# Kernel tuning notes

Measured on AMD Instinct MI355X. Metric: run time of the kernel, lower is better.

Reference implementation:

```python
import jax, jax.numpy as jnp
import numpy as np


def setup_inputs() -> dict:
    key = jax.random.key(0)
    k1, k2 = jax.random.split(key)
    d_feat, n, out_dim = 4096, 8192, 2048
    x = jax.random.normal(k1, (d_feat, n), dtype=jnp.float32)
    Psi = jax.random.normal(k2, (out_dim, n), dtype=jnp.float32)
    return {"x": x, "Psi": Psi}


def reference(x, Psi):
    # Original: out = Psi @ H @ x.T @ x with H = I_n - (1/n) * ones(n, n).
    # Psi @ H subtracts the row-mean of Psi (centering over the sample axis),
    # which is mathematically identical but avoids materializing the n x n H.
    Psi_c = Psi - jnp.mean(Psi, axis=1, keepdims=True)        # [out_dim, n]
    tmp = jnp.einsum('on,dn->od', Psi_c, x)                   # Psi_c @ x.T -> [out_dim, d]
    out = jnp.einsum('od,dn->on', tmp, x)                     # @ x -> [out_dim, n]
    return out
```

## Files before the change

### kernel.cpp

```cpp
#include <hip/hip_runtime.h>
#include <cstdint>
#include <cstddef>


typedef __bf16 bf16x8 __attribute__((ext_vector_type(8)));
typedef float f32x4 __attribute__((ext_vector_type(4)));

__device__ __forceinline__ unsigned short f2bf(float f) {
  unsigned u = __builtin_bit_cast(unsigned, f);
  u += 0x7FFFu + ((u >> 16) & 1u);
  return (unsigned short)(u >> 16);
}

__device__ __forceinline__ void gload_lds16(const void* g, void* l) {
  __builtin_amdgcn_global_load_lds(
      (const __attribute__((address_space(1))) unsigned int*)g,
      (__attribute__((address_space(3))) unsigned int*)l, 16, 0, 0);
}

__device__ __forceinline__ void barrier_nofence() {
  asm volatile("" ::: "memory");
  __builtin_amdgcn_s_barrier();
  asm volatile("" ::: "memory");
}
#define WAIT_LGKM0()                                   \
  do {                                                 \
    asm volatile("s_waitcnt lgkmcnt(0)" ::: "memory"); \
    __builtin_amdgcn_sched_barrier(0);                 \
  } while (0)

template <int MH, int NH, int MFR2>
__device__ __forceinline__ void mma_quad(f32x4 (&acc)[2 * MFR2][4],
                                         const bf16x8 (&aF)[MFR2][2],
                                         const bf16x8 (&bF)[2][2]) {
#pragma unroll
  for (int f = 0; f < MFR2; ++f)
#pragma unroll
    for (int g = 0; g < 2; ++g)
#pragma unroll
      for (int kk = 0; kk < 2; ++kk)
        acc[MH * MFR2 + f][NH * 2 + g] = __builtin_amdgcn_mfma_f32_16x16x32_bf16(
            aF[f][kk], bF[g][kk], acc[MH * MFR2 + f][NH * 2 + g], 0, 0, 0);
}

template <int BM, typename OutT>
__global__ __launch_bounds__(512, 2) void gemm8p(
    const unsigned short* __restrict__ A, const unsigned short* __restrict__ B,
    OutT* __restrict__ C, int M, int Nc, int K) {
  constexpr int BN = 256, BK = 64;
  constexpr int MFR = BM / 32, MFR2 = MFR / 2;
  constexpr int APLANE = BM * 64;
  constexpr int ABUF = 2 * APLANE;
  constexpr int BPLANE = BN * 64, BBUF = 2 * BPLANE;
  __shared__ __align__(1024) char lds[2 * ABUF + 2 * BBUF];
  char* Al = lds;
  char* Bl = lds + 2 * ABUF;

  const int nwg = gridDim.x * gridDim.y;
  const int wgid = blockIdx.y * gridDim.x + blockIdx.x;
  const int swz = (wgid & 7) * (nwg >> 3) + (wgid >> 3);
  const int bx = swz % gridDim.x, by = swz / gridDim.x;
  const int tileM = by * BM, tileN = bx * BN;

  const int t = threadIdx.x, lane = t & 63, wave = t >> 6;
  const int wm = wave >> 2, wn = wave & 3;
  const int rsel = lane & 15;
  const int cs = (((lane >> 4) ^ (((lane >> 3) & 1) << 1)) << 4);

  const unsigned short* Ag = A + (size_t)tileM * K;
  const unsigned short* Bg = B + (size_t)tileN * K;
  const int cgA = (((t & 3) ^ (((t >> 5) & 1) << 1))) * 8;
  const int NT = K / BK;

  auto stageA = [&](int h, int kt) {
    int b2 = kt & 1;
    if constexpr (BM == 256) {
#pragma unroll
      for (int kk = 0; kk < 2; ++kk) {
        int r = h * 128 + (t >> 2);
        gload_lds16(Ag + (size_t)r * K + kt * 64 + kk * 32 + cgA,
                    Al + b2 * ABUF + kk * APLANE + h * 8192 + t * 16);
      }
    } else {
      int r = h * 64 + ((t >> 2) & 63);
      int kk = t >> 8;
      gload_lds16(Ag + (size_t)r * K + kt * 64 + kk * 32 + cgA,
                  Al + b2 * ABUF + kk * APLANE + h * 4096 + (t & 255) * 16);
    }
  };
  auto stageB = [&](int h, int kt) {
    int b2 = kt & 1;
#pragma unroll
    for (int kk = 0; kk < 2; ++kk) {
      int r = h * 128 + (t >> 2);
      gload_lds16(Bg + (size_t)r * K + kt * 64 + kk * 32 + cgA,
                  Bl + b2 * BBUF + kk * BPLANE + h * 8192 + t * 16);
    }
  };
  auto waitv_steady = [&]() {
    if constexpr (BM == 256)
      asm volatile("s_waitcnt vmcnt(6)" ::: "memory");
    else
      asm volatile("s_waitcnt vmcnt(4)" ::: "memory");
  };

  f32x4 acc[MFR][4] = {};
  bf16x8 aF[MFR2][2], bF[2][2];

  stageA(0, 0); stageB(1, 0); stageA(1, 0); stageB(0, 0);
  stageA(0, 1); stageB(1, 1); stageA(1, 1);
  waitv_steady();
  barrier_nofence();

  for (int kt = 0; kt < NT; ++kt) {
    const char* Ab = Al + (kt & 1) * ABUF;
    const char* Bb = Bl + (kt & 1) * BBUF;
#pragma unroll
    for (int f = 0; f < MFR2; ++f)
#pragma unroll
      for (int kk = 0; kk < 2; ++kk)
        aF[f][kk] = *(const bf16x8*)(Ab + kk * APLANE +
                                     ((2 * f + wm) * 16 + rsel) * 64 + cs);
#pragma unroll
    for (int g = 0; g < 2; ++g)
#pragma unroll
      for (int kk = 0; kk < 2; ++kk)
        bF[g][kk] = *(const bf16x8*)(Bb + kk * BPLANE +
                                     ((4 * g + wn) * 16 + rsel) * 64 + cs);
    if (kt + 1 < NT) stageB(0, kt + 1);
    barrier_nofence();
    WAIT_LGKM0();
    __builtin_amdgcn_s_setprio(1);
    mma_quad<0, 0, MFR2>(acc, aF, bF);
    __builtin_amdgcn_s_setprio(0);
    barrier_nofence();
#pragma unroll
    for (int g = 0; g < 2; ++g)
#pragma unroll
      for (int kk = 0; kk < 2; ++kk)
        bF[g][kk] = *(const bf16x8*)(Bb + kk * BPLANE +
                                     ((4 * (g + 2) + wn) * 16 + rsel) * 64 + cs);
    if (kt + 2 < NT) stageA(0, kt + 2);
    barrier_nofence();
    WAIT_LGKM0();
    __builtin_amdgcn_s_setprio(1);
    mma_quad<0, 1, MFR2>(acc, aF, bF);
    __builtin_amdgcn_s_setprio(0);
    barrier_nofence();
#pragma unroll
    for (int f = 0; f < MFR2; ++f)
#pragma unroll
      for (int kk = 0; kk < 2; ++kk)
        aF[f][kk] = *(const bf16x8*)(Ab + kk * APLANE +
                                     ((2 * (f + MFR2) + wm) * 16 + rsel) * 64 + cs);
    if (kt + 2 < NT) stageB(1, kt + 2);
    barrier_nofence();
    WAIT_LGKM0();
    __builtin_amdgcn_s_setprio(1);
    mma_quad<1, 1, MFR2>(acc, aF, bF);
    __builtin_amdgcn_s_setprio(0);
    barrier_nofence();
#pragma unroll
    for (int g = 0; g < 2; ++g)
#pragma unroll
      for (int kk = 0; kk < 2; ++kk)
        bF[g][kk] = *(const bf16x8*)(Bb + kk * BPLANE +
                                     ((4 * g + wn) * 16 + rsel) * 64 + cs);
    if (kt + 2 < NT) stageA(1, kt + 2);
    barrier_nofence();
    WAIT_LGKM0();
    __builtin_amdgcn_s_setprio(1);
    mma_quad<1, 0, MFR2>(acc, aF, bF);
    __builtin_amdgcn_s_setprio(0);
    if (kt + 2 < NT)
      waitv_steady();
    else
      asm volatile("s_waitcnt vmcnt(0)" ::: "memory");
    barrier_nofence();
  }

#pragma unroll
  for (int f = 0; f < MFR; ++f) {
    int row0 = tileM + (2 * f + wm) * 16 + ((lane >> 4) << 2);
#pragma unroll
    for (int g = 0; g < 4; ++g) {
      int col = tileN + (4 * g + wn) * 16 + rsel;
#pragma unroll
      for (int r = 0; r < 4; ++r) {
        size_t off = (size_t)(row0 + r) * Nc + col;
        if constexpr (__is_same(OutT, float))
          C[off] = acc[f][g][r];
        else
          C[off] = f2bf(acc[f][g][r]);
      }
    }
  }
}

__global__ void center_psi_kernel(const float* __restrict__ Psi,
                                  unsigned short* __restrict__ pc, int N) {
  int row = blockIdx.x;
  const float4* src = (const float4*)(Psi + (size_t)row * N);
  int n4 = N >> 2;
  float s = 0.f;
  for (int i = threadIdx.x; i < n4; i += blockDim.x) {
    float4 v = src[i];
    s += (v.x + v.y) + (v.z + v.w);
  }
#pragma unroll
  for (int off = 32; off > 0; off >>= 1) s += __shfl_down(s, off);
  __shared__ float red[4];
  if ((threadIdx.x & 63) == 0) red[threadIdx.x >> 6] = s;
  __syncthreads();
  float mean = (red[0] + red[1] + red[2] + red[3]) / (float)N;
  ushort4* dst = (ushort4*)(pc + (size_t)row * N);
  for (int i = threadIdx.x; i < n4; i += blockDim.x) {
    float4 v = src[i];
    ushort4 o;
    o.x = f2bf(v.x - mean);
    o.y = f2bf(v.y - mean);
    o.z = f2bf(v.z - mean);
    o.w = f2bf(v.w - mean);
    dst[i] = o;
  }
}

__global__ void ct_kernel(const float* __restrict__ x,
                          unsigned short* __restrict__ xb,
                          unsigned short* __restrict__ xtb, int D, int N) {
  __shared__ float tile[64][65];
  int n0 = blockIdx.x * 64, d0 = blockIdx.y * 64;
  int tx = threadIdx.x, ty = threadIdx.y;
#pragma unroll
  for (int i = 0; i < 16; i++) {
    int d = ty + 4 * i;
    float v = x[(size_t)(d0 + d) * N + n0 + tx];
    tile[d][tx] = v;
    xb[(size_t)(d0 + d) * N + n0 + tx] = f2bf(v);
  }
  __syncthreads();
#pragma unroll
  for (int i = 0; i < 16; i++) {
    int nn = ty + 4 * i;
    xtb[(size_t)(n0 + nn) * D + d0 + tx] = f2bf(tile[tx][nn]);
  }
}

extern "C" void kernel_launch(void* const* d_in, const int* in_sizes, int n_in,
                              void* d_out, int out_size, void* d_ws,
                              size_t ws_size, hipStream_t stream) {
  const int D = 4096, N = 8192, O = 2048;
  const float* x = (const float*)d_in[0];
  const float* Psi = (const float*)d_in[1];
  float* out = (float*)d_out;

  char* ws = (char*)d_ws;
  unsigned short* xb = (unsigned short*)(ws);
  unsigned short* xtb = (unsigned short*)(ws + ((size_t)64 << 20));
  unsigned short* pc = (unsigned short*)(ws + ((size_t)128 << 20));
  unsigned short* tmpb = (unsigned short*)(ws + ((size_t)160 << 20));

  center_psi_kernel<<<O, 256, 0, stream>>>(Psi, pc, N);
  ct_kernel<<<dim3(N / 64, D / 64), dim3(64, 4), 0, stream>>>(x, xb, xtb, D, N);
  gemm8p<128, unsigned short><<<dim3(D / 256, O / 128), 512, 0, stream>>>(
      pc, xb, tmpb, O, D, N);
  gemm8p<256, float><<<dim3(N / 256, O / 256), 512, 0, stream>>>(
      tmpb, xtb, out, O, N, D);
}
```

Before: 523.9 us.

## Fuse preprocessing kernels and restructure both GEMM pipelines

Merges the Psi-centering and the x cast/transpose kernels into a single launch. The transpose now uses float4 loads and a bf16 LDS tile. The first GEMM becomes a 2-phase schedule: it loads all B fragments at once and prefetches the full next k-tile, replacing the 4-phase scheme with its two-ahead A prefetch. The second GEMM is specialized into separate bF0/bF1 fragment registers and reuses bF0 in the last quadrant without an extra LDS read. The changes cut launch count, preprocessing memory traffic and LDS reads, at the cost of higher register pressure and a shallower prefetch in the first GEMM.

```diff
diff --git a/kernel.cpp b/kernel.cpp
--- a/kernel.cpp
+++ b/kernel.cpp
@@ -28,29 +28,13 @@
     asm volatile("s_waitcnt lgkmcnt(0)" ::: "memory"); \
     __builtin_amdgcn_sched_barrier(0);                 \
   } while (0)
-
-template <int MH, int NH, int MFR2>
-__device__ __forceinline__ void mma_quad(f32x4 (&acc)[2 * MFR2][4],
-                                         const bf16x8 (&aF)[MFR2][2],
-                                         const bf16x8 (&bF)[2][2]) {
-#pragma unroll
-  for (int f = 0; f < MFR2; ++f)
-#pragma unroll
-    for (int g = 0; g < 2; ++g)
-#pragma unroll
-      for (int kk = 0; kk < 2; ++kk)
-        acc[MH * MFR2 + f][NH * 2 + g] = __builtin_amdgcn_mfma_f32_16x16x32_bf16(
-            aF[f][kk], bF[g][kk], acc[MH * MFR2 + f][NH * 2 + g], 0, 0, 0);
-}
-
-template <int BM, typename OutT>
-__global__ __launch_bounds__(512, 2) void gemm8p(
+#define WAITV(N) asm volatile("s_waitcnt vmcnt(" #N ")" ::: "memory")
+
+__global__ __launch_bounds__(512, 2) void gemm2p(
     const unsigned short* __restrict__ A, const unsigned short* __restrict__ B,
-    OutT* __restrict__ C, int M, int Nc, int K) {
-  constexpr int BN = 256, BK = 64;
-  constexpr int MFR = BM / 32, MFR2 = MFR / 2;
-  constexpr int APLANE = BM * 64;
-  constexpr int ABUF = 2 * APLANE;
+    unsigned short* __restrict__ C, int M, int Nc, int K) {
+  constexpr int BM = 128, BN = 256;
+  constexpr int APLANE = BM * 64, ABUF = 2 * APLANE;
   constexpr int BPLANE = BN * 64, BBUF = 2 * BPLANE;
   __shared__ __align__(1024) char lds[2 * ABUF + 2 * BBUF];
   char* Al = lds;
@@ -70,23 +54,14 @@
   const unsigned short* Ag = A + (size_t)tileM * K;
   const unsigned short* Bg = B + (size_t)tileN * K;
   const int cgA = (((t & 3) ^ (((t >> 5) & 1) << 1))) * 8;
-  const int NT = K / BK;
+  const int NT = K / 64;
 
   auto stageA = [&](int h, int kt) {
     int b2 = kt & 1;
-    if constexpr (BM == 256) {
-#pragma unroll
-      for (int kk = 0; kk < 2; ++kk) {
-        int r = h * 128 + (t >> 2);
-        gload_lds16(Ag + (size_t)r * K + kt * 64 + kk * 32 + cgA,
-                    Al + b2 * ABUF + kk * APLANE + h * 8192 + t * 16);
-      }
-    } else {
-      int r = h * 64 + ((t >> 2) & 63);
-      int kk = t >> 8;
-      gload_lds16(Ag + (size_t)r * K + kt * 64 + kk * 32 + cgA,
-                  Al + b2 * ABUF + kk * APLANE + h * 4096 + (t & 255) * 16);
-    }
+    int r = h * 64 + ((t >> 2) & 63);
+    int kk = t >> 8;
+    gload_lds16(Ag + (size_t)r * K + kt * 64 + kk * 32 + cgA,
+                Al + b2 * ABUF + kk * APLANE + h * 4096 + (t & 255) * 16);
   };
   auto stageB = [&](int h, int kt) {
     int b2 = kt & 1;
@@ -97,152 +72,286 @@
                   Bl + b2 * BBUF + kk * BPLANE + h * 8192 + t * 16);
     }
   };
-  auto waitv_steady = [&]() {
-    if constexpr (BM == 256)
-      asm volatile("s_waitcnt vmcnt(6)" ::: "memory");
-    else
-      asm volatile("s_waitcnt vmcnt(4)" ::: "memory");
-  };
-
-  f32x4 acc[MFR][4] = {};
-  bf16x8 aF[MFR2][2], bF[2][2];
-
-  stageA(0, 0); stageB(1, 0); stageA(1, 0); stageB(0, 0);
-  stageA(0, 1); stageB(1, 1); stageA(1, 1);
-  waitv_steady();
+
+  f32x4 acc[4][4] = {};
+  bf16x8 aF[2][2], bFall[4][2];
+
+  stageB(0, 0); stageA(0, 0); stageB(1, 0); stageA(1, 0);
+  WAITV(1);
   barrier_nofence();
 
   for (int kt = 0; kt < NT; ++kt) {
     const char* Ab = Al + (kt & 1) * ABUF;
     const char* Bb = Bl + (kt & 1) * BBUF;
 #pragma unroll
-    for (int f = 0; f < MFR2; ++f)
+    for (int f = 0; f < 2; ++f)
 #pragma unroll
       for (int kk = 0; kk < 2; ++kk)
         aF[f][kk] = *(const bf16x8*)(Ab + kk * APLANE +
                                      ((2 * f + wm) * 16 + rsel) * 64 + cs);
 #pragma unroll
-    for (int g = 0; g < 2; ++g)
-#pragma unroll
-      for (int kk = 0; kk < 2; ++kk)
-        bF[g][kk] = *(const bf16x8*)(Bb + kk * BPLANE +
-                                     ((4 * g + wn) * 16 + rsel) * 64 + cs);
-    if (kt + 1 < NT) stageB(0, kt + 1);
-    barrier_nofence();
-    WAIT_LGKM0();
-    __builtin_amdgcn_s_setprio(1);
-    mma_quad<0, 0, MFR2>(acc, aF, bF);
-    __builtin_amdgcn_s_setprio(0);
-    barrier_nofence();
-#pragma unroll
-    for (int g = 0; g < 2; ++g)
-#pragma unroll
-      for (int kk = 0; kk < 2; ++kk)
-        bF[g][kk] = *(const bf16x8*)(Bb + kk * BPLANE +
-                                     ((4 * (g + 2) + wn) * 16 + rsel) * 64 + cs);
-    if (kt + 2 < NT) stageA(0, kt + 2);
-    barrier_nofence();
-    WAIT_LGKM0();
-    __builtin_amdgcn_s_setprio(1);
-    mma_quad<0, 1, MFR2>(acc, aF, bF);
-    __builtin_amdgcn_s_setprio(0);
-    barrier_nofence();
-#pragma unroll
-    for (int f = 0; f < MFR2; ++f)
+    for (int g = 0; g < 4; ++g)
+#pragma unroll
+      for (int kk = 0; kk < 2; ++kk)
+        bFall[g][kk] = *(const bf16x8*)(Bb + kk * BPLANE +
+                                        ((4 * g + wn) * 16 + rsel) * 64 + cs);
+    if (kt + 1 < NT) { stageB(0, kt + 1); stageA(0, kt + 1); }
+    barrier_nofence();
+    WAIT_LGKM0();
+    __builtin_amdgcn_s_setprio(1);
+#pragma unroll
+    for (int f = 0; f < 2; ++f)
+#pragma unroll
+      for (int g = 0; g < 4; ++g)
+#pragma unroll
+        for (int kk = 0; kk < 2; ++kk)
+          acc[f][g] = __builtin_amdgcn_mfma_f32_16x16x32_bf16(
+              aF[f][kk], bFall[g][kk], acc[f][g], 0, 0, 0);
+    __builtin_amdgcn_s_setprio(0);
+    if (kt == NT - 1) { WAITV(0); } else { WAITV(3); }
+    barrier_nofence();
+#pragma unroll
+    for (int f = 0; f < 2; ++f)
 #pragma unroll
       for (int kk = 0; kk < 2; ++kk)
         aF[f][kk] = *(const bf16x8*)(Ab + kk * APLANE +
-                                     ((2 * (f + MFR2) + wm) * 16 + rsel) * 64 + cs);
-    if (kt + 2 < NT) stageB(1, kt + 2);
-    barrier_nofence();
-    WAIT_LGKM0();
-    __builtin_amdgcn_s_setprio(1);
-    mma_quad<1, 1, MFR2>(acc, aF, bF);
-    __builtin_amdgcn_s_setprio(0);
-    barrier_nofence();
-#pragma unroll
-    for (int g = 0; g < 2; ++g)
-#pragma unroll
-      for (int kk = 0; kk < 2; ++kk)
-        bF[g][kk] = *(const bf16x8*)(Bb + kk * BPLANE +
-                                     ((4 * g + wn) * 16 + rsel) * 64 + cs);
-    if (kt + 2 < NT) stageA(1, kt + 2);
-    barrier_nofence();
-    WAIT_LGKM0();
-    __builtin_amdgcn_s_setprio(1);
-    mma_quad<1, 0, MFR2>(acc, aF, bF);
-    __builtin_amdgcn_s_setprio(0);
-    if (kt + 2 < NT)
-      waitv_steady();
-    else
-      asm volatile("s_waitcnt vmcnt(0)" ::: "memory");
-    barrier_nofence();
-  }
-
-#pragma unroll
-  for (int f = 0; f < MFR; ++f) {
+                                     ((2 * (f + 2) + wm) * 16 + rsel) * 64 + cs);
+    if (kt + 1 < NT) { stageB(1, kt + 1); stageA(1, kt + 1); }
+    barrier_nofence();
+    WAIT_LGKM0();
+    __builtin_amdgcn_s_setprio(1);
+#pragma unroll
+    for (int f = 0; f < 2; ++f)
+#pragma unroll
+      for (int g = 0; g < 4; ++g)
+#pragma unroll
+        for (int kk = 0; kk < 2; ++kk)
+          acc[2 + f][g] = __builtin_amdgcn_mfma_f32_16x16x32_bf16(
+              aF[f][kk], bFall[g][kk], acc[2 + f][g], 0, 0, 0);
+    __builtin_amdgcn_s_setprio(0);
+    WAITV(1);
+    barrier_nofence();
+  }
+
+#pragma unroll
+  for (int f = 0; f < 4; ++f) {
     int row0 = tileM + (2 * f + wm) * 16 + ((lane >> 4) << 2);
 #pragma unroll
     for (int g = 0; g < 4; ++g) {
       int col = tileN + (4 * g + wn) * 16 + rsel;
 #pragma unroll
-      for (int r = 0; r < 4; ++r) {
-        size_t off = (size_t)(row0 + r) * Nc + col;
-        if constexpr (__is_same(OutT, float))
-          C[off] = acc[f][g][r];
-        else
-          C[off] = f2bf(acc[f][g][r]);
-      }
-    }
-  }
-}
-
-__global__ void center_psi_kernel(const float* __restrict__ Psi,
-                                  unsigned short* __restrict__ pc, int N) {
-  int row = blockIdx.x;
-  const float4* src = (const float4*)(Psi + (size_t)row * N);
-  int n4 = N >> 2;
-  float s = 0.f;
-  for (int i = threadIdx.x; i < n4; i += blockDim.x) {
-    float4 v = src[i];
-    s += (v.x + v.y) + (v.z + v.w);
-  }
-#pragma unroll
-  for (int off = 32; off > 0; off >>= 1) s += __shfl_down(s, off);
+      for (int r = 0; r < 4; ++r)
+        C[(size_t)(row0 + r) * Nc + col] = f2bf(acc[f][g][r]);
+    }
+  }
+}
+
+__global__ __launch_bounds__(512, 2) void gemm4p(
+    const unsigned short* __restrict__ A, const unsigned short* __restrict__ B,
+    float* __restrict__ C, int M, int Nc, int K) {
+  constexpr int BM = 256, BN = 256;
+  constexpr int APLANE = BM * 64, ABUF = 2 * APLANE;
+  constexpr int BPLANE = BN * 64, BBUF = 2 * BPLANE;
+  __shared__ __align__(1024) char lds[2 * ABUF + 2 * BBUF];
+  char* Al = lds;
+  char* Bl = lds + 2 * ABUF;
+
+  const int nwg = gridDim.x * gridDim.y;
+  const int wgid = blockIdx.y * gridDim.x + blockIdx.x;
+  const int swz = (wgid & 7) * (nwg >> 3) + (wgid >> 3);
+  const int bx = swz % gridDim.x, by = swz / gridDim.x;
+  const int tileM = by * BM, tileN = bx * BN;
+
+  const int t = threadIdx.x, lane = t & 63, wave = t >> 6;
+  const int wm = wave >> 2, wn = wave & 3;
+  const int rsel = lane & 15;
+  const int cs = (((lane >> 4) ^ (((lane >> 3) & 1) << 1)) << 4);
+
+  const unsigned short* Ag = A + (size_t)tileM * K;
+  const unsigned short* Bg = B + (size_t)tileN * K;
+  const int cgA = (((t & 3) ^ (((t >> 5) & 1) << 1))) * 8;
+  const int NT = K / 64;
+
+  auto stageA = [&](int h, int kt) {
+    int b2 = kt & 1;
+#pragma unroll
+    for (int kk = 0; kk < 2; ++kk) {
+      int r = h * 128 + (t >> 2);
+      gload_lds16(Ag + (size_t)r * K + kt * 64 + kk * 32 + cgA,
+                  Al + b2 * ABUF + kk * APLANE + h * 8192 + t * 16);
+    }
+  };
+  auto stageB = [&](int h, int kt) {
+    int b2 = kt & 1;
+#pragma unroll
+    for (int kk = 0; kk < 2; ++kk) {
+      int r = h * 128 + (t >> 2);
+      gload_lds16(Bg + (size_t)r * K + kt * 64 + kk * 32 + cgA,
+                  Bl + b2 * BBUF + kk * BPLANE + h * 8192 + t * 16);
+    }
+  };
+
+  f32x4 acc[8][4] = {};
+  bf16x8 aF[4][2], bF0[2][2], bF1[2][2];
+
+  stageA(0, 0); stageB(1, 0); stageA(1, 0); stageB(0, 0);
+  stageA(0, 1); stageB(1, 1); stageA(1, 1);
+  WAITV(6);
+  barrier_nofence();
+
+  for (int kt = 0; kt < NT; ++kt) {
+    const char* Ab = Al + (kt & 1) * ABUF;
+    const char* Bb = Bl + (kt & 1) * BBUF;
+#pragma unroll
+    for (int f = 0; f < 4; ++f)
+#pragma unroll
+      for (int kk = 0; kk < 2; ++kk)
+        aF[f][kk] = *(const bf16x8*)(Ab + kk * APLANE +
+                                     ((2 * f + wm) * 16 + rsel) * 64 + cs);
+#pragma unroll
+    for (int g = 0; g < 2; ++g)
+#pragma unroll
+      for (int kk = 0; kk < 2; ++kk)
+        bF0[g][kk] = *(const bf16x8*)(Bb + kk * BPLANE +
+                                      ((4 * g + wn) * 16 + rsel) * 64 + cs);
+    if (kt + 1 < NT) stageB(0, kt + 1);
+    barrier_nofence();
+    WAIT_LGKM0();
+    __builtin_amdgcn_s_setprio(1);
+#pragma unroll
+    for (int f = 0; f < 4; ++f)
+#pragma unroll
+      for (int g = 0; g < 2; ++g)
+#pragma unroll
+        for (int kk = 0; kk < 2; ++kk)
+          acc[f][g] = __builtin_amdgcn_mfma_f32_16x16x32_bf16(
+              aF[f][kk], bF0[g][kk], acc[f][g], 0, 0, 0);
+    __builtin_amdgcn_s_setprio(0);
+    barrier_nofence();
+#pragma unroll
+    for (int g = 0; g < 2; ++g)
+#pragma unroll
+      for (int kk = 0; kk < 2; ++kk)
+        bF1[g][kk] = *(const bf16x8*)(Bb + kk * BPLANE +
+                                      ((4 * (g + 2) + wn) * 16 + rsel) * 64 + cs);
+    if (kt + 2 < NT) stageA(0, kt + 2);
+    barrier_nofence();
+    WAIT_LGKM0();
+    __builtin_amdgcn_s_setprio(1);
+#pragma unroll
+    for (int f = 0; f < 4; ++f)
+#pragma unroll
+      for (int g = 0; g < 2; ++g)
+#pragma unroll
+        for (int kk = 0; kk < 2; ++kk)
+          acc[f][2 + g] = __builtin_amdgcn_mfma_f32_16x16x32_bf16(
+              aF[f][kk], bF1[g][kk], acc[f][2 + g], 0, 0, 0);
+    __builtin_amdgcn_s_setprio(0);
+    barrier_nofence();
+#pragma unroll
+    for (int f = 0; f < 4; ++f)
+#pragma unroll
+      for (int kk = 0; kk < 2; ++kk)
+        aF[f][kk] = *(const bf16x8*)(Ab + kk * APLANE +
+                                     ((2 * (f + 4) + wm) * 16 + rsel) * 64 + cs);
+    if (kt + 2 < NT) stageB(1, kt + 2);
+    barrier_nofence();
+    WAIT_LGKM0();
+    __builtin_amdgcn_s_setprio(1);
+#pragma unroll
+    for (int f = 0; f < 4; ++f)
+#pragma unroll
+      for (int g = 0; g < 2; ++g)
+#pragma unroll
+        for (int kk = 0; kk < 2; ++kk)
+          acc[4 + f][2 + g] = __builtin_amdgcn_mfma_f32_16x16x32_bf16(
+              aF[f][kk], bF1[g][kk], acc[4 + f][2 + g], 0, 0, 0);
+    __builtin_amdgcn_s_setprio(0);
+    barrier_nofence();
+    if (kt + 2 < NT) stageA(1, kt + 2);
+    __builtin_amdgcn_s_setprio(1);
+#pragma unroll
+    for (int f = 0; f < 4; ++f)
+#pragma unroll
+      for (int g = 0; g < 2; ++g)
+#pragma unroll
+        for (int kk = 0; kk < 2; ++kk)
+          acc[4 + f][g] = __builtin_amdgcn_mfma_f32_16x16x32_bf16(
+              aF[f][kk], bF0[g][kk], acc[4 + f][g], 0, 0, 0);
+    __builtin_amdgcn_s_setprio(0);
+    if (kt + 2 < NT) { WAITV(6); } else { WAITV(0); }
+    barrier_nofence();
+  }
+
+#pragma unroll
+  for (int f = 0; f < 8; ++f) {
+    int row0 = tileM + (2 * f + wm) * 16 + ((lane >> 4) << 2);
+#pragma unroll
+    for (int g = 0; g < 4; ++g) {
+      int col = tileN + (4 * g + wn) * 16 + rsel;
+#pragma unroll
+      for (int r = 0; r < 4; ++r)
+        C[(size_t)(row0 + r) * Nc + col] = acc[f][g][r];
+    }
+  }
+}
+
+__global__ void pre_kernel(const float* __restrict__ x,
+                           const float* __restrict__ Psi,
+                           unsigned short* __restrict__ xb,
+                           unsigned short* __restrict__ xtb,
+                           unsigned short* __restrict__ pc, int D, int N) {
+  __shared__ unsigned short tileT[64][66];
   __shared__ float red[4];
-  if ((threadIdx.x & 63) == 0) red[threadIdx.x >> 6] = s;
-  __syncthreads();
-  float mean = (red[0] + red[1] + red[2] + red[3]) / (float)N;
-  ushort4* dst = (ushort4*)(pc + (size_t)row * N);
-  for (int i = threadIdx.x; i < n4; i += blockDim.x) {
-    float4 v = src[i];
-    ushort4 o;
-    o.x = f2bf(v.x - mean);
-    o.y = f2bf(v.y - mean);
-    o.z = f2bf(v.z - mean);
-    o.w = f2bf(v.w - mean);
-    dst[i] = o;
-  }
-}
-
-__global__ void ct_kernel(const float* __restrict__ x,
-                          unsigned short* __restrict__ xb,
-                          unsigned short* __restrict__ xtb, int D, int N) {
-  __shared__ float tile[64][65];
-  int n0 = blockIdx.x * 64, d0 = blockIdx.y * 64;
-  int tx = threadIdx.x, ty = threadIdx.y;
-#pragma unroll
-  for (int i = 0; i < 16; i++) {
-    int d = ty + 4 * i;
-    float v = x[(size_t)(d0 + d) * N + n0 + tx];
-    tile[d][tx] = v;
-    xb[(size_t)(d0 + d) * N + n0 + tx] = f2bf(v);
-  }
-  __syncthreads();
-#pragma unroll
-  for (int i = 0; i < 16; i++) {
-    int nn = ty + 4 * i;
-    xtb[(size_t)(n0 + nn) * D + d0 + tx] = f2bf(tile[tx][nn]);
+  const int bid = blockIdx.x, t = threadIdx.x;
+  if (bid < 8192) {
+    const int n0 = (bid & 127) * 64, d0 = (bid >> 7) * 64;
+    const int tx = t & 15, ty = t >> 4;
+#pragma unroll
+    for (int dy = 0; dy < 4; ++dy) {
+      int d = ty + 16 * dy;
+      float4 v = *(const float4*)(x + (size_t)(d0 + d) * N + n0 + tx * 4);
+      ushort4 o;
+      o.x = f2bf(v.x); o.y = f2bf(v.y); o.z = f2bf(v.z); o.w = f2bf(v.w);
+      *(ushort4*)(xb + (size_t)(d0 + d) * N + n0 + tx * 4) = o;
+      tileT[tx * 4 + 0][d] = o.x;
+      tileT[tx * 4 + 1][d] = o.y;
+      tileT[tx * 4 + 2][d] = o.z;
+      tileT[tx * 4 + 3][d] = o.w;
+    }
+    __syncthreads();
+#pragma unroll
+    for (int ny = 0; ny < 4; ++ny) {
+      int n = ty + 16 * ny;
+      ushort2 a = *(const ushort2*)&tileT[n][tx * 4];
+      ushort2 b = *(const ushort2*)&tileT[n][tx * 4 + 2];
+      ushort4 o; o.x = a.x; o.y = a.y; o.z = b.x; o.w = b.y;
+      *(ushort4*)(xtb + (size_t)(n0 + n) * D + d0 + tx * 4) = o;
+    }
+  } else {
+    const int row = bid - 8192;
+    const float4* src = (const float4*)(Psi + (size_t)row * N);
+    int n4 = N >> 2;
+    float s = 0.f;
+    for (int i = t; i < n4; i += blockDim.x) {
+      float4 v = src[i];
+      s += (v.x + v.y) + (v.z + v.w);
+    }
+#pragma unroll
+    for (int off = 32; off > 0; off >>= 1) s += __shfl_down(s, off);
+    if ((t & 63) == 0) red[t >> 6] = s;
+    __syncthreads();
+    float mean = (red[0] + red[1] + red[2] + red[3]) / (float)N;
+    ushort4* dst = (ushort4*)(pc + (size_t)row * N);
+    for (int i = t; i < n4; i += blockDim.x) {
+      float4 v = src[i];
+      ushort4 o;
+      o.x = f2bf(v.x - mean);
+      o.y = f2bf(v.y - mean);
+      o.z = f2bf(v.z - mean);
+      o.w = f2bf(v.w - mean);
+      dst[i] = o;
+    }
   }
 }
 
@@ -260,10 +369,7 @@
   unsigned short* pc = (unsigned short*)(ws + ((size_t)128 << 20));
   unsigned short* tmpb = (unsigned short*)(ws + ((size_t)160 << 20));
 
-  center_psi_kernel<<<O, 256, 0, stream>>>(Psi, pc, N);
-  ct_kernel<<<dim3(N / 64, D / 64), dim3(64, 4), 0, stream>>>(x, xb, xtb, D, N);
-  gemm8p<128, unsigned short><<<dim3(D / 256, O / 128), 512, 0, stream>>>(
-      pc, xb, tmpb, O, D, N);
-  gemm8p<256, float><<<dim3(N / 256, O / 256), 512, 0, stream>>>(
-      tmpb, xtb, out, O, N, D);
-}
+  pre_kernel<<<8192 + O, 256, 0, stream>>>(x, Psi, xb, xtb, pc, D, N);
+  gemm2p<<<dim3(D / 256, O / 128), 512, 0, stream>>>(pc, xb, tmpb, O, D, N);
+  gemm4p<<<dim3(N / 256, O / 256), 512, 0, stream>>>(tmpb, xtb, out, O, N, D);
+}
```

Result: slower. 560.7 us (+7.0%).
